# Kernel tuning notes

Measured on AMD Instinct MI355X. Metric: run time of the kernel, lower is better.

The kernel has to match this reference:

```python
import jax, jax.numpy as jnp
import numpy as np

B, HQ, HKV, D = 32, 32, 8, 128
BLOCK_SIZE, MAX_BLOCKS = 16, 128
NUM_BLOCKS = B * MAX_BLOCKS
LMAX = MAX_BLOCKS * BLOCK_SIZE  # 2048 max context per sequence
ROPE_BASE = 10000.0


def _rope(x, pos):
    """Apply rotary embedding. x: [B, H, D], pos: [B] int positions."""
    half = D // 2
    inv_freq = 1.0 / (ROPE_BASE ** (jnp.arange(0, D, 2, dtype=jnp.float32) / D))  # [D/2]
    freqs = pos.astype(jnp.float32)[:, None] * inv_freq[None, :]  # [B, D/2]
    emb = jnp.concatenate([freqs, freqs], axis=-1)                # [B, D]
    cos = jnp.cos(emb)[:, None, :]  # [B, 1, D]
    sin = jnp.sin(emb)[:, None, :]
    x1, x2 = x[..., :half], x[..., half:]
    rotated = jnp.concatenate([-x2, x1], axis=-1)
    return x * cos + rotated * sin


def setup_inputs() -> dict:
    key = jax.random.key(0)
    ks = jax.random.split(key, 6)
    query = jax.random.normal(ks[0], (B, HQ, D), jnp.float32)
    new_k = jax.random.normal(ks[1], (B, HKV, D), jnp.float32)
    new_v = jax.random.normal(ks[2], (B, HKV, D), jnp.float32)
    k_cache = jax.random.normal(ks[3], (NUM_BLOCKS, BLOCK_SIZE, HKV, D), jnp.float32)
    v_cache = jax.random.normal(ks[4], (NUM_BLOCKS, BLOCK_SIZE, HKV, D), jnp.float32)
    # each sequence owns a disjoint contiguous range of blocks
    block_table = jnp.arange(B * MAX_BLOCKS, dtype=jnp.int32).reshape(B, MAX_BLOCKS)
    context_lens = jax.random.randint(ks[5], (B,), 1, LMAX - 1).astype(jnp.int32)
    return dict(query=query, new_k=new_k, new_v=new_v, k_cache=k_cache,
                v_cache=v_cache, block_table=block_table, context_lens=context_lens)


def reference(query, new_k, new_v, k_cache, v_cache, block_table, context_lens):
    scale = 1.0 / D ** 0.5
    pos = context_lens  # new token position for each sequence, [B]

    # RoPE on the decode-step query and key (seq_len == 1 per sequence)
    q = _rope(query, pos)      # [B, HQ, D]
    k_new = _rope(new_k, pos)  # [B, HKV, D]

    # flatten paged cache to [NUM_BLOCKS*BLOCK_SIZE, HKV, D]
    kc = k_cache.reshape(-1, HKV, D)
    vc = v_cache.reshape(-1, HKV, D)

    # paged KV-cache append: slot = block_table[b, pos//bs]*bs + pos%bs
    blk_new = jnp.take_along_axis(block_table, (pos // BLOCK_SIZE)[:, None], axis=1)[:, 0]
    slot = blk_new * BLOCK_SIZE + pos % BLOCK_SIZE  # [B]
    kc = kc.at[slot].set(k_new)
    vc = vc.at[slot].set(new_v)

    # gather per-sequence K/V via block table: [B, LMAX, HKV, D]
    p = jnp.arange(LMAX, dtype=jnp.int32)
    blks = block_table[:, p // BLOCK_SIZE]                 # [B, LMAX]
    idx = blks * BLOCK_SIZE + (p % BLOCK_SIZE)[None, :]    # [B, LMAX]
    keys = kc[idx]
    vals = vc[idx]

    # GQA attention over valid context (lengths = context_lens + 1 after append)
    lens = pos + 1
    g = HQ // HKV
    qg = q.reshape(B, HKV, g, D)
    scores = jnp.einsum('bkgd,blkd->bkgl', qg, keys) * scale  # [B, HKV, g, LMAX]
    mask = p[None, :] < lens[:, None]  # [B, LMAX]
    scores = jnp.where(mask[:, None, None, :], scores, -jnp.inf)
    w = jax.nn.softmax(scores, axis=-1)
    out = jnp.einsum('bkgl,blkd->bkgd', w, vals)
    return out.reshape(B, HQ, D)
```

## Files before the change

kernel.cpp:

```cpp
#include <hip/hip_runtime.h>
#include <math.h>

#define BATCH 32
#define HQ 32
#define HKV 8
#define DHEAD 128
#define BS 16
#define MAXB 128
#define G 4
#define CHUNK 256
#define MAXCH 8
#define NW 4
#define NT (NW * 64)

#define NSLOT (BATCH * HKV * MAXCH)
#define NBKV  (BATCH * HKV)

typedef float v2f __attribute__((ext_vector_type(2)));

__device__ __forceinline__ v2f pk_fma(v2f a, v2f b, v2f c) {
    v2f d;
    asm("v_pk_fma_f32 %0, %1, %2, %3" : "=v"(d) : "v"(a), "v"(b), "v"(c));
    return d;
}
__device__ __forceinline__ v2f pk_mul(v2f a, v2f b) {
    v2f d;
    asm("v_pk_mul_f32 %0, %1, %2" : "=v"(d) : "v"(a), "v"(b));
    return d;
}
__device__ __forceinline__ float fexp2(float x) {
    float r;
    asm("v_exp_f32 %0, %1" : "=v"(r) : "v"(x));
    return r;
}

#define ROR4(N, x0, x1, x2, x3)                                                   \
    asm("s_nop 1\n\t"                                                             \
        "v_add_f32_dpp %0, %0, %0 row_ror:" #N " row_mask:0xf bank_mask:0xf\n\t"  \
        "v_add_f32_dpp %1, %1, %1 row_ror:" #N " row_mask:0xf bank_mask:0xf\n\t"  \
        "v_add_f32_dpp %2, %2, %2 row_ror:" #N " row_mask:0xf bank_mask:0xf\n\t"  \
        "v_add_f32_dpp %3, %3, %3 row_ror:" #N " row_mask:0xf bank_mask:0xf"      \
        : "+v"(x0), "+v"(x1), "+v"(x2), "+v"(x3))

__global__ __launch_bounds__(128) void paged_attn_prep(
    const float* __restrict__ query,
    const int*   __restrict__ context_lens,
    float* __restrict__ qs)
{
    const int bkv = blockIdx.x;
    const int kv  = bkv & 7;
    const int b   = bkv >> 3;
    const int tid = threadIdx.x;

    __shared__ float s_cos[64], s_sin[64];
    const int pos = context_lens[b];
    if (tid < 64) {
        float invf = exp2f((float)tid * -0.20762050593046014f);
        float ang  = (float)pos * invf;
        s_cos[tid] = cosf(ang);
        s_sin[tid] = sinf(ang);
    }
    __syncthreads();

    const float scale = 0.08838834764831845f * 1.4426950408889634f;

    for (int idx = tid; idx < G * DHEAD; idx += 128) {
        int h = idx >> 7, d = idx & 127;
        const float* qp = query + ((size_t)b * HQ + kv * G + h) * DHEAD;
        float x = qp[d], r;
        if (d < 64) r = x * s_cos[d]      - qp[d + 64] * s_sin[d];
        else        r = x * s_cos[d - 64] + qp[d - 64] * s_sin[d - 64];
        qs[(size_t)bkv * (G * DHEAD) + idx] = r * scale;
    }
}

__global__ __launch_bounds__(NT) void paged_attn_chunk(
    const float* __restrict__ k_cache,
    const float* __restrict__ v_cache,
    const int*   __restrict__ block_table,
    const int*   __restrict__ context_lens,
    const float* __restrict__ qs,
    float*       __restrict__ wsacc,
    float*       __restrict__ wsl)
{
    const int c   = blockIdx.x & (MAXCH - 1);
    const int bkv = blockIdx.x >> 3;
    const int kv  = bkv & 7;
    const int b   = bkv >> 3;

    const int pos = context_lens[b];
    const int c0  = c << 8;
    if (c0 > pos) return;

    const int tid  = threadIdx.x;
    const int w    = tid >> 6;
    const int lane = tid & 63;
    const int grp  = lane >> 4;
    const int sub  = lane & 15;

    __shared__ float s_wacc[NW][G][DHEAD];
    __shared__ float s_wl[NW][G];

    v2f q2[G][4];
    const float* qb = qs + (size_t)bkv * (G * DHEAD) + sub * 8;
    #pragma unroll
    for (int h = 0; h < G; h++) {
        float4 qa = *(const float4*)(qb + h * DHEAD);
        float4 qc = *(const float4*)(qb + h * DHEAD + 4);
        q2[h][0] = v2f{qa.x, qa.y}; q2[h][1] = v2f{qa.z, qa.w};
        q2[h][2] = v2f{qc.x, qc.y}; q2[h][3] = v2f{qc.z, qc.w};
    }

    const int tb  = b * MAXB + (c0 >> 4) + w * 4;
    const int bt0 = __builtin_amdgcn_readfirstlane(block_table[tb + 0]);
    const int bt1 = __builtin_amdgcn_readfirstlane(block_table[tb + 1]);
    const int bt2 = __builtin_amdgcn_readfirstlane(block_table[tb + 2]);
    const int bt3 = __builtin_amdgcn_readfirstlane(block_table[tb + 3]);

    const size_t BLKF = (size_t)BS * HKV * DHEAD;
    const int loff = grp * (HKV * DHEAD) + kv * DHEAD + sub * 8;

    const float* kparr[4] = { k_cache + bt0 * BLKF + loff,
                              k_cache + bt1 * BLKF + loff,
                              k_cache + bt2 * BLKF + loff,
                              k_cache + bt3 * BLKF + loff };
    const float* vparr[4] = { v_cache + bt0 * BLKF + loff,
                              v_cache + bt1 * BLKF + loff,
                              v_cache + bt2 * BLKF + loff,
                              v_cache + bt3 * BLKF + loff };

    const int p0 = c0 + w * 64 + grp;

    v2f acc2[G][4];
    float l[G];
    #pragma unroll
    for (int h = 0; h < G; h++) {
        l[h] = 0.f;
        #pragma unroll
        for (int j = 0; j < 4; j++) acc2[h][j] = v2f{0.f, 0.f};
    }

    float4 kaA, kbA, vaA, vbA;
    float4 kaB, kbB, vaB, vbB;

#define LOADSET(KA, KB, VA, VB, IT) do {                                       \
        const float* kp_ = kparr[(IT) >> 2] + ((IT) & 3) * (4 * HKV * DHEAD);  \
        const float* vp_ = vparr[(IT) >> 2] + ((IT) & 3) * (4 * HKV * DHEAD);  \
        KA = *(const float4*)kp_;  KB = *(const float4*)(kp_ + 4);             \
        VA = *(const float4*)vp_;  VB = *(const float4*)(vp_ + 4);             \
    } while (0)

#define COMPSET(KA, KB, VA, VB, IT) do {                                       \
        const int pi_ = p0 + (IT) * 4;                                         \
        v2f k0_ = v2f{KA.x, KA.y}, k1_ = v2f{KA.z, KA.w};                      \
        v2f k2_ = v2f{KB.x, KB.y}, k3_ = v2f{KB.z, KB.w};                      \
        v2f d0_ = pk_fma(q2[0][3], k3_, pk_fma(q2[0][2], k2_,                  \
                  pk_fma(q2[0][1], k1_, pk_mul(q2[0][0], k0_))));              \
        v2f d1_ = pk_fma(q2[1][3], k3_, pk_fma(q2[1][2], k2_,                  \
                  pk_fma(q2[1][1], k1_, pk_mul(q2[1][0], k0_))));              \
        v2f d2_ = pk_fma(q2[2][3], k3_, pk_fma(q2[2][2], k2_,                  \
                  pk_fma(q2[2][1], k1_, pk_mul(q2[2][0], k0_))));              \
        v2f d3_ = pk_fma(q2[3][3], k3_, pk_fma(q2[3][2], k2_,                  \
                  pk_fma(q2[3][1], k1_, pk_mul(q2[3][0], k0_))));              \
        float dt0 = d0_.x + d0_.y, dt1 = d1_.x + d1_.y;                        \
        float dt2 = d2_.x + d2_.y, dt3 = d3_.x + d3_.y;                        \
        ROR4(8, dt0, dt1, dt2, dt3);                                           \
        ROR4(4, dt0, dt1, dt2, dt3);                                           \
        ROR4(2, dt0, dt1, dt2, dt3);                                           \
        ROR4(1, dt0, dt1, dt2, dt3);                                           \
        const bool act_ = pi_ < pos;        \
        float wg0 = act_ ? fexp2(dt0) : 0.f;                                   \
        float wg1 = act_ ? fexp2(dt1) : 0.f;                                   \
        float wg2 = act_ ? fexp2(dt2) : 0.f;                                   \
        float wg3 = act_ ? fexp2(dt3) : 0.f;                                   \
        l[0] += wg0; l[1] += wg1; l[2] += wg2; l[3] += wg3;                    \
        v2f u0_ = v2f{VA.x, VA.y}, u1_ = v2f{VA.z, VA.w};                      \
        v2f u2_ = v2f{VB.x, VB.y}, u3_ = v2f{VB.z, VB.w};                      \
        v2f w0_ = v2f{wg0, wg0}, w1_ = v2f{wg1, wg1};                          \
        v2f w2_ = v2f{wg2, wg2}, w3_ = v2f{wg3, wg3};                          \
        acc2[0][0] = pk_fma(w0_, u0_, acc2[0][0]);                             \
        acc2[0][1] = pk_fma(w0_, u1_, acc2[0][1]);                             \
        acc2[0][2] = pk_fma(w0_, u2_, acc2[0][2]);                             \
        acc2[0][3] = pk_fma(w0_, u3_, acc2[0][3]);                             \
        acc2[1][0] = pk_fma(w1_, u0_, acc2[1][0]);                             \
        acc2[1][1] = pk_fma(w1_, u1_, acc2[1][1]);                             \
        acc2[1][2] = pk_fma(w1_, u2_, acc2[1][2]);                             \
        acc2[1][3] = pk_fma(w1_, u3_, acc2[1][3]);                             \
        acc2[2][0] = pk_fma(w2_, u0_, acc2[2][0]);                             \
        acc2[2][1] = pk_fma(w2_, u1_, acc2[2][1]);                             \
        acc2[2][2] = pk_fma(w2_, u2_, acc2[2][2]);                             \
        acc2[2][3] = pk_fma(w2_, u3_, acc2[2][3]);                             \
        acc2[3][0] = pk_fma(w3_, u0_, acc2[3][0]);                             \
        acc2[3][1] = pk_fma(w3_, u1_, acc2[3][1]);                             \
        acc2[3][2] = pk_fma(w3_, u2_, acc2[3][2]);                             \
        acc2[3][3] = pk_fma(w3_, u3_, acc2[3][3]);                             \
    } while (0)

    LOADSET(kaA, kbA, vaA, vbA, 0);
    LOADSET(kaB, kbB, vaB, vbB, 1);
    COMPSET(kaA, kbA, vaA, vbA, 0);   LOADSET(kaA, kbA, vaA, vbA, 2);
    COMPSET(kaB, kbB, vaB, vbB, 1);   LOADSET(kaB, kbB, vaB, vbB, 3);
    COMPSET(kaA, kbA, vaA, vbA, 2);   LOADSET(kaA, kbA, vaA, vbA, 4);
    COMPSET(kaB, kbB, vaB, vbB, 3);   LOADSET(kaB, kbB, vaB, vbB, 5);
    COMPSET(kaA, kbA, vaA, vbA, 4);   LOADSET(kaA, kbA, vaA, vbA, 6);
    COMPSET(kaB, kbB, vaB, vbB, 5);   LOADSET(kaB, kbB, vaB, vbB, 7);
    COMPSET(kaA, kbA, vaA, vbA, 6);   LOADSET(kaA, kbA, vaA, vbA, 8);
    COMPSET(kaB, kbB, vaB, vbB, 7);   LOADSET(kaB, kbB, vaB, vbB, 9);
    COMPSET(kaA, kbA, vaA, vbA, 8);   LOADSET(kaA, kbA, vaA, vbA, 10);
    COMPSET(kaB, kbB, vaB, vbB, 9);   LOADSET(kaB, kbB, vaB, vbB, 11);
    COMPSET(kaA, kbA, vaA, vbA, 10);  LOADSET(kaA, kbA, vaA, vbA, 12);
    COMPSET(kaB, kbB, vaB, vbB, 11);  LOADSET(kaB, kbB, vaB, vbB, 13);
    COMPSET(kaA, kbA, vaA, vbA, 12);  LOADSET(kaA, kbA, vaA, vbA, 14);
    COMPSET(kaB, kbB, vaB, vbB, 13);  LOADSET(kaB, kbB, vaB, vbB, 15);
    COMPSET(kaA, kbA, vaA, vbA, 14);
    COMPSET(kaB, kbB, vaB, vbB, 15);

#undef LOADSET
#undef COMPSET

    #pragma unroll
    for (int h = 0; h < G; h++) {
        l[h] += __shfl_xor(l[h], 16, 64);
        l[h] += __shfl_xor(l[h], 32, 64);
        #pragma unroll
        for (int j = 0; j < 4; j++) {
            float ax = acc2[h][j].x, ay = acc2[h][j].y;
            ax += __shfl_xor(ax, 16, 64); ax += __shfl_xor(ax, 32, 64);
            ay += __shfl_xor(ay, 16, 64); ay += __shfl_xor(ay, 32, 64);
            acc2[h][j] = v2f{ax, ay};
        }
    }
    if (lane < 16) {
        #pragma unroll
        for (int h = 0; h < G; h++)
            #pragma unroll
            for (int j = 0; j < 4; j++) {
                s_wacc[w][h][sub * 8 + 2 * j]     = acc2[h][j].x;
                s_wacc[w][h][sub * 8 + 2 * j + 1] = acc2[h][j].y;
            }
    }
    if (lane == 0) {
        #pragma unroll
        for (int h = 0; h < G; h++) s_wl[w][h] = l[h];
    }
    __syncthreads();

    const size_t slot_base = (size_t)blockIdx.x * (G * DHEAD);
    for (int idx = tid; idx < G * DHEAD; idx += NT) {
        float s = s_wacc[0][idx >> 7][idx & 127] + s_wacc[1][idx >> 7][idx & 127]
                + s_wacc[2][idx >> 7][idx & 127] + s_wacc[3][idx >> 7][idx & 127];
        wsacc[slot_base + idx] = s;
    }
    if (tid < G) {
        wsl[(size_t)blockIdx.x * G + tid] =
            s_wl[0][tid] + s_wl[1][tid] + s_wl[2][tid] + s_wl[3][tid];
    }
}

__global__ __launch_bounds__(512) void paged_attn_combine(
    const float* __restrict__ new_k,
    const float* __restrict__ new_v,
    const int*   __restrict__ context_lens,
    const float* __restrict__ qs,
    const float* __restrict__ wsacc,
    const float* __restrict__ wsl,
    float*       __restrict__ out)
{
    const int bkv = blockIdx.x;
    const int kv  = bkv & 7;
    const int b   = bkv >> 3;
    const int t   = threadIdx.x;
    const int h   = t >> 7;
    const int d   = t & 127;
    const int wv  = t >> 6;

    __shared__ float s_cos[64], s_sin[64], s_kn[DHEAD], s_ps[8];

    const int pos = context_lens[b];
    if (t < 64) {
        float invf = exp2f((float)t * -0.20762050593046014f);
        float ang  = (float)pos * invf;
        s_cos[t] = cosf(ang);
        s_sin[t] = sinf(ang);
    }
    __syncthreads();
    if (t < DHEAD) {
        const float* kp = new_k + ((size_t)b * HKV + kv) * DHEAD;
        float x = kp[t], r;
        if (t < 64) r = x * s_cos[t]      - kp[t + 64] * s_sin[t];
        else        r = x * s_cos[t - 64] + kp[t - 64] * s_sin[t - 64];
        s_kn[t] = r;
    }
    __syncthreads();

    float part = qs[(size_t)bkv * (G * DHEAD) + t] * s_kn[d];
    #pragma unroll
    for (int off = 1; off < 64; off <<= 1) part += __shfl_xor(part, off, 64);
    if ((t & 63) == 0) s_ps[wv] = part;
    __syncthreads();

    const float wnew = fexp2(s_ps[2 * h] + s_ps[2 * h + 1]);

    const int len = pos + 1;
    const int nch = (len + CHUNK - 1) >> 8;

    float asum = 0.f, lsum = 0.f;
    for (int cc = 0; cc < nch; cc++) {
        asum += wsacc[((size_t)bkv * MAXCH + cc) * (G * DHEAD) + t];
        lsum += wsl[((size_t)bkv * MAXCH + cc) * G + h];
    }
    const float vnew = new_v[((size_t)b * HKV + kv) * DHEAD + d];
    out[((size_t)b * HQ + kv * G + h) * DHEAD + d] =
        (asum + wnew * vnew) / (lsum + wnew);
}

extern "C" void kernel_launch(void* const* d_in, const int* in_sizes, int n_in,
                              void* d_out, int out_size, void* d_ws, size_t ws_size,
                              hipStream_t stream) {
    const float* query        = (const float*)d_in[0];
    const float* new_k        = (const float*)d_in[1];
    const float* new_v        = (const float*)d_in[2];
    const float* k_cache      = (const float*)d_in[3];
    const float* v_cache      = (const float*)d_in[4];
    const int*   block_table  = (const int*)d_in[5];
    const int*   context_lens = (const int*)d_in[6];
    float* out = (float*)d_out;

    float* wsacc = (float*)d_ws;
    float* wsl   = wsacc + (size_t)NSLOT * G * DHEAD;
    float* qs    = wsl + (size_t)NSLOT * G;

    paged_attn_prep<<<dim3(NBKV), dim3(128), 0, stream>>>(
        query, context_lens, qs);
    paged_attn_chunk<<<dim3(NSLOT), dim3(NT), 0, stream>>>(
        k_cache, v_cache, block_table, context_lens, qs, wsacc, wsl);
    paged_attn_combine<<<dim3(NBKV), dim3(512), 0, stream>>>(
        new_k, new_v, context_lens, qs, wsacc, wsl, out);
}
```

Before: 79.72 us.

## Fuse query RoPE prep into chunk kernel, skip inactive blocks, use nontemporal loads

Drops the separate query-prep kernel. Each chunk block and the combine kernel now recompute the rotated, scaled query themselves, which removes one launch and a workspace round trip. The chunk kernel skips whole 16-token cache blocks past the context length, and loads K/V with nontemporal loads in two half-batches instead of the previous double-buffered software pipeline. The cost is redundant RoPE and trig work in every chunk block, plus possibly less load/compute overlap.

Result: slower. 87.34 us (+9.6%).

```diff
diff --git a/kernel.cpp b/kernel.cpp
--- a/kernel.cpp
+++ b/kernel.cpp
@@ -11,12 +11,15 @@
 #define CHUNK 256
 #define MAXCH 8
 #define NW 4
-#define NT (NW * 64)
-
+#define NTHR (NW * 64)
 #define NSLOT (BATCH * HKV * MAXCH)
 #define NBKV  (BATCH * HKV)
+#define BLKF  (BS * HKV * DHEAD)
+
+#define SCALE_LOG2E 0.12752740305928724f
 
 typedef float v2f __attribute__((ext_vector_type(2)));
+typedef float v4f __attribute__((ext_vector_type(4)));
 
 __device__ __forceinline__ v2f pk_fma(v2f a, v2f b, v2f c) {
     v2f d;
@@ -32,6 +35,9 @@
     float r;
     asm("v_exp_f32 %0, %1" : "=v"(r) : "v"(x));
     return r;
+}
+__device__ __forceinline__ v4f ntload(const float* p) {
+    return __builtin_nontemporal_load((const v4f*)p);
 }
 
 #define ROR4(N, x0, x1, x2, x3)                                                   \
@@ -42,44 +48,12 @@
         "v_add_f32_dpp %3, %3, %3 row_ror:" #N " row_mask:0xf bank_mask:0xf"      \
         : "+v"(x0), "+v"(x1), "+v"(x2), "+v"(x3))
 
-__global__ __launch_bounds__(128) void paged_attn_prep(
+__global__ __launch_bounds__(NTHR) void paged_attn_chunk(
     const float* __restrict__ query,
-    const int*   __restrict__ context_lens,
-    float* __restrict__ qs)
-{
-    const int bkv = blockIdx.x;
-    const int kv  = bkv & 7;
-    const int b   = bkv >> 3;
-    const int tid = threadIdx.x;
-
-    __shared__ float s_cos[64], s_sin[64];
-    const int pos = context_lens[b];
-    if (tid < 64) {
-        float invf = exp2f((float)tid * -0.20762050593046014f);
-        float ang  = (float)pos * invf;
-        s_cos[tid] = cosf(ang);
-        s_sin[tid] = sinf(ang);
-    }
-    __syncthreads();
-
-    const float scale = 0.08838834764831845f * 1.4426950408889634f;
-
-    for (int idx = tid; idx < G * DHEAD; idx += 128) {
-        int h = idx >> 7, d = idx & 127;
-        const float* qp = query + ((size_t)b * HQ + kv * G + h) * DHEAD;
-        float x = qp[d], r;
-        if (d < 64) r = x * s_cos[d]      - qp[d + 64] * s_sin[d];
-        else        r = x * s_cos[d - 64] + qp[d - 64] * s_sin[d - 64];
-        qs[(size_t)bkv * (G * DHEAD) + idx] = r * scale;
-    }
-}
-
-__global__ __launch_bounds__(NT) void paged_attn_chunk(
     const float* __restrict__ k_cache,
     const float* __restrict__ v_cache,
     const int*   __restrict__ block_table,
     const int*   __restrict__ context_lens,
-    const float* __restrict__ qs,
     float*       __restrict__ wsacc,
     float*       __restrict__ wsl)
 {
@@ -90,7 +64,7 @@
 
     const int pos = context_lens[b];
     const int c0  = c << 8;
-    if (c0 > pos) return;
+    if (c0 >= pos) return;
 
     const int tid  = threadIdx.x;
     const int w    = tid >> 6;
@@ -98,132 +72,143 @@
     const int grp  = lane >> 4;
     const int sub  = lane & 15;
 
+    __shared__ float s_cos[64], s_sin[64];
+    __shared__ float s_q[G * DHEAD];
     __shared__ float s_wacc[NW][G][DHEAD];
     __shared__ float s_wl[NW][G];
 
+    if (tid < 64) {
+        float invf = exp2f((float)tid * -0.20762050593046014f);
+        float ang  = (float)pos * invf;
+        s_cos[tid] = cosf(ang);
+        s_sin[tid] = sinf(ang);
+    }
+    __syncthreads();
+
+    for (int idx = tid; idx < G * DHEAD; idx += NTHR) {
+        int h = idx >> 7, d = idx & 127;
+        const float* qp = query + ((size_t)b * HQ + kv * G + h) * DHEAD;
+        float x = qp[d], r;
+        if (d < 64) r = x * s_cos[d]      - qp[d + 64] * s_sin[d];
+        else        r = x * s_cos[d - 64] + qp[d - 64] * s_sin[d - 64];
+        s_q[idx] = r * SCALE_LOG2E;
+    }
+    __syncthreads();
+
     v2f q2[G][4];
-    const float* qb = qs + (size_t)bkv * (G * DHEAD) + sub * 8;
     #pragma unroll
-    for (int h = 0; h < G; h++) {
-        float4 qa = *(const float4*)(qb + h * DHEAD);
-        float4 qc = *(const float4*)(qb + h * DHEAD + 4);
+    for (int h = 0; h < G; ++h) {
+        float4 qa = *(const float4*)&s_q[h * DHEAD + sub * 8];
+        float4 qc = *(const float4*)&s_q[h * DHEAD + sub * 8 + 4];
         q2[h][0] = v2f{qa.x, qa.y}; q2[h][1] = v2f{qa.z, qa.w};
         q2[h][2] = v2f{qc.x, qc.y}; q2[h][3] = v2f{qc.z, qc.w};
     }
 
-    const int tb  = b * MAXB + (c0 >> 4) + w * 4;
+    int a = pos - (c0 + w * 64);
+    a = a < 0 ? 0 : (a > 64 ? 64 : a);
+
+    const int tb  = b * MAXB + c * 16 + w * 4;
     const int bt0 = __builtin_amdgcn_readfirstlane(block_table[tb + 0]);
     const int bt1 = __builtin_amdgcn_readfirstlane(block_table[tb + 1]);
     const int bt2 = __builtin_amdgcn_readfirstlane(block_table[tb + 2]);
     const int bt3 = __builtin_amdgcn_readfirstlane(block_table[tb + 3]);
 
-    const size_t BLKF = (size_t)BS * HKV * DHEAD;
     const int loff = grp * (HKV * DHEAD) + kv * DHEAD + sub * 8;
-
-    const float* kparr[4] = { k_cache + bt0 * BLKF + loff,
-                              k_cache + bt1 * BLKF + loff,
-                              k_cache + bt2 * BLKF + loff,
-                              k_cache + bt3 * BLKF + loff };
-    const float* vparr[4] = { v_cache + bt0 * BLKF + loff,
-                              v_cache + bt1 * BLKF + loff,
-                              v_cache + bt2 * BLKF + loff,
-                              v_cache + bt3 * BLKF + loff };
-
-    const int p0 = c0 + w * 64 + grp;
+    const float* kb0 = k_cache + (size_t)bt0 * BLKF + loff;
+    const float* kb1 = k_cache + (size_t)bt1 * BLKF + loff;
+    const float* kb2 = k_cache + (size_t)bt2 * BLKF + loff;
+    const float* kb3 = k_cache + (size_t)bt3 * BLKF + loff;
+    const float* vb0 = v_cache + (size_t)bt0 * BLKF + loff;
+    const float* vb1 = v_cache + (size_t)bt1 * BLKF + loff;
+    const float* vb2 = v_cache + (size_t)bt2 * BLKF + loff;
+    const float* vb3 = v_cache + (size_t)bt3 * BLKF + loff;
 
     v2f acc2[G][4];
     float l[G];
     #pragma unroll
-    for (int h = 0; h < G; h++) {
+    for (int h = 0; h < G; ++h) {
         l[h] = 0.f;
         #pragma unroll
-        for (int j = 0; j < 4; j++) acc2[h][j] = v2f{0.f, 0.f};
-    }
-
-    float4 kaA, kbA, vaA, vbA;
-    float4 kaB, kbB, vaB, vbB;
-
-#define LOADSET(KA, KB, VA, VB, IT) do {                                       \
-        const float* kp_ = kparr[(IT) >> 2] + ((IT) & 3) * (4 * HKV * DHEAD);  \
-        const float* vp_ = vparr[(IT) >> 2] + ((IT) & 3) * (4 * HKV * DHEAD);  \
-        KA = *(const float4*)kp_;  KB = *(const float4*)(kp_ + 4);             \
-        VA = *(const float4*)vp_;  VB = *(const float4*)(vp_ + 4);             \
+        for (int j = 0; j < 4; ++j) acc2[h][j] = v2f{0.f, 0.f};
+    }
+
+#define CBLOCK(KB, VB, CBI)                                                    \
+    do {                                                                       \
+        _Pragma("unroll")                                                      \
+        for (int hb = 0; hb < 2; ++hb) {                                       \
+            v4f kk[4], vv[4];                                                  \
+            _Pragma("unroll")                                                  \
+            for (int i2 = 0; i2 < 2; ++i2) {                                   \
+                const int it2 = hb * 2 + i2;                                   \
+                kk[2*i2]   = ntload((KB) + it2 * 4096);                        \
+                kk[2*i2+1] = ntload((KB) + it2 * 4096 + 4);                    \
+                vv[2*i2]   = ntload((VB) + it2 * 4096);                        \
+                vv[2*i2+1] = ntload((VB) + it2 * 4096 + 4);                    \
+            }                                                                  \
+            _Pragma("unroll")                                                  \
+            for (int i2 = 0; i2 < 2; ++i2) {                                   \
+                const int it2 = hb * 2 + i2;                                   \
+                const int pi_ = c0 + w * 64 + (CBI) * 16 + it2 * 4 + grp;      \
+                v2f k0_ = v2f{kk[2*i2].x, kk[2*i2].y};                         \
+                v2f k1_ = v2f{kk[2*i2].z, kk[2*i2].w};                         \
+                v2f k2_ = v2f{kk[2*i2+1].x, kk[2*i2+1].y};                     \
+                v2f k3_ = v2f{kk[2*i2+1].z, kk[2*i2+1].w};                     \
+                v2f d0_ = pk_fma(q2[0][3], k3_, pk_fma(q2[0][2], k2_,          \
+                          pk_fma(q2[0][1], k1_, pk_mul(q2[0][0], k0_))));      \
+                v2f d1_ = pk_fma(q2[1][3], k3_, pk_fma(q2[1][2], k2_,          \
+                          pk_fma(q2[1][1], k1_, pk_mul(q2[1][0], k0_))));      \
+                v2f d2_ = pk_fma(q2[2][3], k3_, pk_fma(q2[2][2], k2_,          \
+                          pk_fma(q2[2][1], k1_, pk_mul(q2[2][0], k0_))));      \
+                v2f d3_ = pk_fma(q2[3][3], k3_, pk_fma(q2[3][2], k2_,          \
+                          pk_fma(q2[3][1], k1_, pk_mul(q2[3][0], k0_))));      \
+                float dt0 = d0_.x + d0_.y, dt1 = d1_.x + d1_.y;                \
+                float dt2 = d2_.x + d2_.y, dt3 = d3_.x + d3_.y;                \
+                ROR4(8, dt0, dt1, dt2, dt3);                                   \
+                ROR4(4, dt0, dt1, dt2, dt3);                                   \
+                ROR4(2, dt0, dt1, dt2, dt3);                                   \
+                ROR4(1, dt0, dt1, dt2, dt3);                                   \
+                const bool act_ = pi_ < pos;                                   \
+                float wg0 = act_ ? fexp2(dt0) : 0.f;                           \
+                float wg1 = act_ ? fexp2(dt1) : 0.f;                           \
+                float wg2 = act_ ? fexp2(dt2) : 0.f;                           \
+                float wg3 = act_ ? fexp2(dt3) : 0.f;                           \
+                l[0] += wg0; l[1] += wg1; l[2] += wg2; l[3] += wg3;            \
+                v2f u0_ = v2f{vv[2*i2].x, vv[2*i2].y};                         \
+                v2f u1_ = v2f{vv[2*i2].z, vv[2*i2].w};                         \
+                v2f u2_ = v2f{vv[2*i2+1].x, vv[2*i2+1].y};                     \
+                v2f u3_ = v2f{vv[2*i2+1].z, vv[2*i2+1].w};                     \
+                acc2[0][0] = pk_fma(v2f{wg0, wg0}, u0_, acc2[0][0]);           \
+                acc2[0][1] = pk_fma(v2f{wg0, wg0}, u1_, acc2[0][1]);           \
+                acc2[0][2] = pk_fma(v2f{wg0, wg0}, u2_, acc2[0][2]);           \
+                acc2[0][3] = pk_fma(v2f{wg0, wg0}, u3_, acc2[0][3]);           \
+                acc2[1][0] = pk_fma(v2f{wg1, wg1}, u0_, acc2[1][0]);           \
+                acc2[1][1] = pk_fma(v2f{wg1, wg1}, u1_, acc2[1][1]);           \
+                acc2[1][2] = pk_fma(v2f{wg1, wg1}, u2_, acc2[1][2]);           \
+                acc2[1][3] = pk_fma(v2f{wg1, wg1}, u3_, acc2[1][3]);           \
+                acc2[2][0] = pk_fma(v2f{wg2, wg2}, u0_, acc2[2][0]);           \
+                acc2[2][1] = pk_fma(v2f{wg2, wg2}, u1_, acc2[2][1]);           \
+                acc2[2][2] = pk_fma(v2f{wg2, wg2}, u2_, acc2[2][2]);           \
+                acc2[2][3] = pk_fma(v2f{wg2, wg2}, u3_, acc2[2][3]);           \
+                acc2[3][0] = pk_fma(v2f{wg3, wg3}, u0_, acc2[3][0]);           \
+                acc2[3][1] = pk_fma(v2f{wg3, wg3}, u1_, acc2[3][1]);           \
+                acc2[3][2] = pk_fma(v2f{wg3, wg3}, u2_, acc2[3][2]);           \
+                acc2[3][3] = pk_fma(v2f{wg3, wg3}, u3_, acc2[3][3]);           \
+            }                                                                  \
+        }                                                                      \
     } while (0)
 
-#define COMPSET(KA, KB, VA, VB, IT) do {                                       \
-        const int pi_ = p0 + (IT) * 4;                                         \
-        v2f k0_ = v2f{KA.x, KA.y}, k1_ = v2f{KA.z, KA.w};                      \
-        v2f k2_ = v2f{KB.x, KB.y}, k3_ = v2f{KB.z, KB.w};                      \
-        v2f d0_ = pk_fma(q2[0][3], k3_, pk_fma(q2[0][2], k2_,                  \
-                  pk_fma(q2[0][1], k1_, pk_mul(q2[0][0], k0_))));              \
-        v2f d1_ = pk_fma(q2[1][3], k3_, pk_fma(q2[1][2], k2_,                  \
-                  pk_fma(q2[1][1], k1_, pk_mul(q2[1][0], k0_))));              \
-        v2f d2_ = pk_fma(q2[2][3], k3_, pk_fma(q2[2][2], k2_,                  \
-                  pk_fma(q2[2][1], k1_, pk_mul(q2[2][0], k0_))));              \
-        v2f d3_ = pk_fma(q2[3][3], k3_, pk_fma(q2[3][2], k2_,                  \
-                  pk_fma(q2[3][1], k1_, pk_mul(q2[3][0], k0_))));              \
-        float dt0 = d0_.x + d0_.y, dt1 = d1_.x + d1_.y;                        \
-        float dt2 = d2_.x + d2_.y, dt3 = d3_.x + d3_.y;                        \
-        ROR4(8, dt0, dt1, dt2, dt3);                                           \
-        ROR4(4, dt0, dt1, dt2, dt3);                                           \
-        ROR4(2, dt0, dt1, dt2, dt3);                                           \
-        ROR4(1, dt0, dt1, dt2, dt3);                                           \
-        const bool act_ = pi_ < pos;        \
-        float wg0 = act_ ? fexp2(dt0) : 0.f;                                   \
-        float wg1 = act_ ? fexp2(dt1) : 0.f;                                   \
-        float wg2 = act_ ? fexp2(dt2) : 0.f;                                   \
-        float wg3 = act_ ? fexp2(dt3) : 0.f;                                   \
-        l[0] += wg0; l[1] += wg1; l[2] += wg2; l[3] += wg3;                    \
-        v2f u0_ = v2f{VA.x, VA.y}, u1_ = v2f{VA.z, VA.w};                      \
-        v2f u2_ = v2f{VB.x, VB.y}, u3_ = v2f{VB.z, VB.w};                      \
-        v2f w0_ = v2f{wg0, wg0}, w1_ = v2f{wg1, wg1};                          \
-        v2f w2_ = v2f{wg2, wg2}, w3_ = v2f{wg3, wg3};                          \
-        acc2[0][0] = pk_fma(w0_, u0_, acc2[0][0]);                             \
-        acc2[0][1] = pk_fma(w0_, u1_, acc2[0][1]);                             \
-        acc2[0][2] = pk_fma(w0_, u2_, acc2[0][2]);                             \
-        acc2[0][3] = pk_fma(w0_, u3_, acc2[0][3]);                             \
-        acc2[1][0] = pk_fma(w1_, u0_, acc2[1][0]);                             \
-        acc2[1][1] = pk_fma(w1_, u1_, acc2[1][1]);                             \
-        acc2[1][2] = pk_fma(w1_, u2_, acc2[1][2]);                             \
-        acc2[1][3] = pk_fma(w1_, u3_, acc2[1][3]);                             \
-        acc2[2][0] = pk_fma(w2_, u0_, acc2[2][0]);                             \
-        acc2[2][1] = pk_fma(w2_, u1_, acc2[2][1]);                             \
-        acc2[2][2] = pk_fma(w2_, u2_, acc2[2][2]);                             \
-        acc2[2][3] = pk_fma(w2_, u3_, acc2[2][3]);                             \
-        acc2[3][0] = pk_fma(w3_, u0_, acc2[3][0]);                             \
-        acc2[3][1] = pk_fma(w3_, u1_, acc2[3][1]);                             \
-        acc2[3][2] = pk_fma(w3_, u2_, acc2[3][2]);                             \
-        acc2[3][3] = pk_fma(w3_, u3_, acc2[3][3]);                             \
-    } while (0)
-
-    LOADSET(kaA, kbA, vaA, vbA, 0);
-    LOADSET(kaB, kbB, vaB, vbB, 1);
-    COMPSET(kaA, kbA, vaA, vbA, 0);   LOADSET(kaA, kbA, vaA, vbA, 2);
-    COMPSET(kaB, kbB, vaB, vbB, 1);   LOADSET(kaB, kbB, vaB, vbB, 3);
-    COMPSET(kaA, kbA, vaA, vbA, 2);   LOADSET(kaA, kbA, vaA, vbA, 4);
-    COMPSET(kaB, kbB, vaB, vbB, 3);   LOADSET(kaB, kbB, vaB, vbB, 5);
-    COMPSET(kaA, kbA, vaA, vbA, 4);   LOADSET(kaA, kbA, vaA, vbA, 6);
-    COMPSET(kaB, kbB, vaB, vbB, 5);   LOADSET(kaB, kbB, vaB, vbB, 7);
-    COMPSET(kaA, kbA, vaA, vbA, 6);   LOADSET(kaA, kbA, vaA, vbA, 8);
-    COMPSET(kaB, kbB, vaB, vbB, 7);   LOADSET(kaB, kbB, vaB, vbB, 9);
-    COMPSET(kaA, kbA, vaA, vbA, 8);   LOADSET(kaA, kbA, vaA, vbA, 10);
-    COMPSET(kaB, kbB, vaB, vbB, 9);   LOADSET(kaB, kbB, vaB, vbB, 11);
-    COMPSET(kaA, kbA, vaA, vbA, 10);  LOADSET(kaA, kbA, vaA, vbA, 12);
-    COMPSET(kaB, kbB, vaB, vbB, 11);  LOADSET(kaB, kbB, vaB, vbB, 13);
-    COMPSET(kaA, kbA, vaA, vbA, 12);  LOADSET(kaA, kbA, vaA, vbA, 14);
-    COMPSET(kaB, kbB, vaB, vbB, 13);  LOADSET(kaB, kbB, vaB, vbB, 15);
-    COMPSET(kaA, kbA, vaA, vbA, 14);
-    COMPSET(kaB, kbB, vaB, vbB, 15);
-
-#undef LOADSET
-#undef COMPSET
+    if (a > 0)  CBLOCK(kb0, vb0, 0);
+    if (a > 16) CBLOCK(kb1, vb1, 1);
+    if (a > 32) CBLOCK(kb2, vb2, 2);
+    if (a > 48) CBLOCK(kb3, vb3, 3);
+#undef CBLOCK
 
     #pragma unroll
-    for (int h = 0; h < G; h++) {
+    for (int h = 0; h < G; ++h) {
         l[h] += __shfl_xor(l[h], 16, 64);
         l[h] += __shfl_xor(l[h], 32, 64);
         #pragma unroll
-        for (int j = 0; j < 4; j++) {
+        for (int j = 0; j < 4; ++j) {
             float ax = acc2[h][j].x, ay = acc2[h][j].y;
             ax += __shfl_xor(ax, 16, 64); ax += __shfl_xor(ax, 32, 64);
             ay += __shfl_xor(ay, 16, 64); ay += __shfl_xor(ay, 32, 64);
@@ -232,21 +217,21 @@
     }
     if (lane < 16) {
         #pragma unroll
-        for (int h = 0; h < G; h++)
+        for (int h = 0; h < G; ++h)
             #pragma unroll
-            for (int j = 0; j < 4; j++) {
+            for (int j = 0; j < 4; ++j) {
                 s_wacc[w][h][sub * 8 + 2 * j]     = acc2[h][j].x;
                 s_wacc[w][h][sub * 8 + 2 * j + 1] = acc2[h][j].y;
             }
     }
     if (lane == 0) {
         #pragma unroll
-        for (int h = 0; h < G; h++) s_wl[w][h] = l[h];
+        for (int h = 0; h < G; ++h) s_wl[w][h] = l[h];
     }
     __syncthreads();
 
     const size_t slot_base = (size_t)blockIdx.x * (G * DHEAD);
-    for (int idx = tid; idx < G * DHEAD; idx += NT) {
+    for (int idx = tid; idx < G * DHEAD; idx += NTHR) {
         float s = s_wacc[0][idx >> 7][idx & 127] + s_wacc[1][idx >> 7][idx & 127]
                 + s_wacc[2][idx >> 7][idx & 127] + s_wacc[3][idx >> 7][idx & 127];
         wsacc[slot_base + idx] = s;
@@ -258,10 +243,10 @@
 }
 
 __global__ __launch_bounds__(512) void paged_attn_combine(
+    const float* __restrict__ query,
     const float* __restrict__ new_k,
     const float* __restrict__ new_v,
     const int*   __restrict__ context_lens,
-    const float* __restrict__ qs,
     const float* __restrict__ wsacc,
     const float* __restrict__ wsl,
     float*       __restrict__ out)
@@ -293,7 +278,15 @@
     }
     __syncthreads();
 
-    float part = qs[(size_t)bkv * (G * DHEAD) + t] * s_kn[d];
+    float rq;
+    {
+        const float* qp = query + ((size_t)b * HQ + kv * G + h) * DHEAD;
+        float x = qp[d];
+        if (d < 64) rq = x * s_cos[d]      - qp[d + 64] * s_sin[d];
+        else        rq = x * s_cos[d - 64] + qp[d - 64] * s_sin[d - 64];
+        rq *= SCALE_LOG2E;
+    }
+    float part = rq * s_kn[d];
     #pragma unroll
     for (int off = 1; off < 64; off <<= 1) part += __shfl_xor(part, off, 64);
     if ((t & 63) == 0) s_ps[wv] = part;
@@ -301,11 +294,10 @@
 
     const float wnew = fexp2(s_ps[2 * h] + s_ps[2 * h + 1]);
 
-    const int len = pos + 1;
-    const int nch = (len + CHUNK - 1) >> 8;
+    const int ncc = (pos + CHUNK - 1) >> 8;
 
     float asum = 0.f, lsum = 0.f;
-    for (int cc = 0; cc < nch; cc++) {
+    for (int cc = 0; cc < ncc; cc++) {
         asum += wsacc[((size_t)bkv * MAXCH + cc) * (G * DHEAD) + t];
         lsum += wsl[((size_t)bkv * MAXCH + cc) * G + h];
     }
@@ -328,12 +320,9 @@
 
     float* wsacc = (float*)d_ws;
     float* wsl   = wsacc + (size_t)NSLOT * G * DHEAD;
-    float* qs    = wsl + (size_t)NSLOT * G;
-
-    paged_attn_prep<<<dim3(NBKV), dim3(128), 0, stream>>>(
-        query, context_lens, qs);
-    paged_attn_chunk<<<dim3(NSLOT), dim3(NT), 0, stream>>>(
-        k_cache, v_cache, block_table, context_lens, qs, wsacc, wsl);
+
+    paged_attn_chunk<<<dim3(NSLOT), dim3(NTHR), 0, stream>>>(
+        query, k_cache, v_cache, block_table, context_lens, wsacc, wsl);
     paged_attn_combine<<<dim3(NBKV), dim3(512), 0, stream>>>(
-        new_k, new_v, context_lens, qs, wsacc, wsl, out);
-}
+        query, new_k, new_v, context_lens, wsacc, wsl, out);
+}
```
